# Kernel optimization log

Measured on AMD Instinct MI355X. Metric: run time of the kernel, lower is better.

Reference implementation:

```python
import jax, jax.numpy as jnp
import numpy as np

D_MODEL = 512
BATCH_A = 8192
MAX_MATCHES = 16
N_B = 100000
D_HID = 2 * D_MODEL  # 1024
D_IN = 2 * D_MODEL   # concat([a, mean_b])


def setup_inputs() -> dict:
    key = jax.random.key(0)
    ks = jax.random.split(key, 10)
    table_a_emb = jax.random.normal(ks[0], (BATCH_A, D_MODEL), dtype=jnp.float32)
    table_b_emb = jax.random.normal(ks[1], (N_B, D_MODEL), dtype=jnp.float32)
    # padded neighbor lists; negative values mark padding / no-match
    match_indices = jax.random.randint(ks[2], (BATCH_A, MAX_MATCHES), -5, N_B, dtype=jnp.int64)
    s_in = 1.0 / np.sqrt(D_IN)
    s_h = 1.0 / np.sqrt(D_HID)
    W_in = jax.random.uniform(ks[3], (D_IN, D_HID), jnp.float32, -s_in, s_in)
    b_in = jax.random.uniform(ks[4], (D_HID,), jnp.float32, -s_in, s_in)
    W_h = jax.random.uniform(ks[5], (D_HID, D_HID), jnp.float32, -s_h, s_h)
    b_h = jax.random.uniform(ks[6], (D_HID,), jnp.float32, -s_h, s_h)
    W_out = jax.random.uniform(ks[7], (D_HID, D_MODEL), jnp.float32, -s_h, s_h)
    b_out = jax.random.uniform(ks[8], (D_MODEL,), jnp.float32, -s_h, s_h)
    return {"table_a_emb": table_a_emb, "table_b_emb": table_b_emb,
            "match_indices": match_indices, "W_in": W_in, "b_in": b_in,
            "W_h": W_h, "b_h": b_h, "W_out": W_out, "b_out": b_out}


def reference(table_a_emb, table_b_emb, match_indices, W_in, b_in, W_h, b_h, W_out, b_out):
    mask = match_indices >= 0                                   # [B, M]
    safe_idx = jnp.where(mask, match_indices, 0)
    gathered = table_b_emb[safe_idx] * mask[..., None].astype(table_b_emb.dtype)  # [B, M, D]
    counts = mask.sum(axis=-1)                                  # [B]
    denom = jnp.maximum(counts, 1).astype(table_b_emb.dtype)[:, None]
    agg_b = gathered.sum(axis=1) / denom                        # [B, D] masked mean
    combined = jnp.concatenate([table_a_emb, agg_b], axis=-1)   # [B, 2D]
    h = jax.nn.relu(combined @ W_in + b_in)
    h = jax.nn.relu(h @ W_h + b_h)
    out = h @ W_out + b_out                                     # [B, D]
    # rows with zero valid matches emit zeros, not MLP(concat(a, 0))
    return jnp.where((counts > 0)[:, None], out, jnp.zeros_like(out))
```

## Files before the change

### kernel.cpp

```cpp
#include <hip/hip_runtime.h>

#define DM 512
#define DI 1024
#define MM 16

typedef __attribute__((ext_vector_type(4))) float f32x4;
typedef __attribute__((ext_vector_type(8))) short short8;
typedef __attribute__((ext_vector_type(8))) unsigned short ushort8;

__device__ __forceinline__ unsigned short f2bf(float x) {
  union { float f; unsigned u; } c; c.f = x;
  unsigned r = (c.u + 0x7fffu + ((c.u >> 16) & 1u)) >> 16;
  return (unsigned short)r;
}

__device__ __forceinline__ void gload_lds16(const void* g, void* l) {
  __builtin_amdgcn_global_load_lds(
      (const __attribute__((address_space(1))) unsigned int*)g,
      (__attribute__((address_space(3))) unsigned int*)l, 16, 0, 0);
}

__global__ void wt_bf16_kernel(const float* __restrict__ W,
                               unsigned short* __restrict__ Wt,
                               int K, int N) {
  __shared__ float tile[32][33];
  int bx = blockIdx.x * 32;
  int by = blockIdx.y * 32;
  int tx = threadIdx.x & 31, ty = threadIdx.x >> 5;
  #pragma unroll
  for (int i = ty; i < 32; i += 8)
    tile[i][tx] = W[(size_t)(by + i) * N + bx + tx];
  __syncthreads();
  #pragma unroll
  for (int i = ty; i < 32; i += 8)
    Wt[(size_t)(bx + i) * K + by + tx] = f2bf(tile[tx][i]);
}

__global__ void build_x_kernel(const float* __restrict__ Aemb,
                               const float* __restrict__ Bemb,
                               const int* __restrict__ midx,
                               unsigned short* __restrict__ X,
                               int* __restrict__ counts) {
  int row = blockIdx.x * 4 + (threadIdx.x >> 6);
  int l = threadIdx.x & 63;
  float acc[8] = {0,0,0,0,0,0,0,0};
  int cnt = 0;
  const int* ip = midx + row * MM;
  #pragma unroll
  for (int m = 0; m < MM; ++m) {
    int id = ip[m];
    if (id >= 0) {
      ++cnt;
      const f32x4* p = (const f32x4*)(Bemb + (size_t)id * DM) + l * 2;
      f32x4 u = p[0], v = p[1];
      acc[0]+=u[0]; acc[1]+=u[1]; acc[2]+=u[2]; acc[3]+=u[3];
      acc[4]+=v[0]; acc[5]+=v[1]; acc[6]+=v[2]; acc[7]+=v[3];
    }
  }
  float inv = 1.0f / (float)(cnt > 0 ? cnt : 1);
  const f32x4* pa = (const f32x4*)(Aemb + (size_t)row * DM) + l * 2;
  f32x4 a0 = pa[0], a1 = pa[1];
  ushort8 va, vb;
  va[0]=f2bf(a0[0]); va[1]=f2bf(a0[1]); va[2]=f2bf(a0[2]); va[3]=f2bf(a0[3]);
  va[4]=f2bf(a1[0]); va[5]=f2bf(a1[1]); va[6]=f2bf(a1[2]); va[7]=f2bf(a1[3]);
  #pragma unroll
  for (int i = 0; i < 8; ++i) vb[i] = f2bf(acc[i] * inv);
  *(ushort8*)(X + (size_t)row * DI + l * 8) = va;
  *(ushort8*)(X + (size_t)row * DI + DM + l * 8) = vb;
  if (l == 0) counts[row] = cnt;
}

template<int RELU, int FINAL>
__global__ __launch_bounds__(256, 2)
void gemm_kernel(const unsigned short* __restrict__ A,
                 const unsigned short* __restrict__ Bt,
                 const float* __restrict__ bias,
                 unsigned short* __restrict__ Cb,
                 float* __restrict__ Cf,
                 const int* __restrict__ counts,
                 int M, int N, int K) {
  __shared__ __align__(16) unsigned short As[128 * 64];
  __shared__ __align__(16) unsigned short Bs[128 * 64];
  const int t = threadIdx.x;
  const int l = t & 63, w = t >> 6;
  const int wr = w >> 1, wc = w & 1;
  const int blockM = blockIdx.y * 128, blockN = blockIdx.x * 128;
  const unsigned short* Ab = A + (size_t)blockM * K;
  const unsigned short* Bb = Bt + (size_t)blockN * K;

  f32x4 acc[4][4];
  #pragma unroll
  for (int m = 0; m < 4; ++m)
    #pragma unroll
    for (int n = 0; n < 4; ++n) acc[m][n] = (f32x4){0.f, 0.f, 0.f, 0.f};

  int so_row[4], so_col[4];
  #pragma unroll
  for (int c = 0; c < 4; ++c) {
    int o = c * 4096 + t * 16;
    int row = o >> 7;
    int cb = (o & 127) ^ ((row & 7) << 4);
    so_row[c] = row; so_col[c] = cb >> 1;
  }

  const int r = l & 15, ko = (l >> 4) * 8;
  const int swz = (r & 7) << 4;
  const char* Ac = (const char*)As;
  const char* Bc = (const char*)Bs;
  const int NT = K >> 6;

  #pragma unroll
  for (int c = 0; c < 4; ++c) {
    gload_lds16(Ab + (size_t)so_row[c] * K + so_col[c], (char*)As + c * 4096 + w * 1024);
    gload_lds16(Bb + (size_t)so_row[c] * K + so_col[c], (char*)Bs + c * 4096 + w * 1024);
  }

  for (int kt = 0; kt < NT; ++kt) {
    __syncthreads();
    #pragma unroll
    for (int kk = 0; kk < 64; kk += 32) {
      short8 aF[4], bF[4];
      #pragma unroll
      for (int m = 0; m < 4; ++m) {
        int byteo = ((wr * 64 + m * 16 + r) * 128 + (kk + ko) * 2) ^ swz;
        aF[m] = *(const short8*)(Ac + byteo);
      }
      #pragma unroll
      for (int n = 0; n < 4; ++n) {
        int byteo = ((wc * 64 + n * 16 + r) * 128 + (kk + ko) * 2) ^ swz;
        bF[n] = *(const short8*)(Bc + byteo);
      }
      #pragma unroll
      for (int m = 0; m < 4; ++m)
        #pragma unroll
        for (int n = 0; n < 4; ++n)
          acc[m][n] = __builtin_amdgcn_mfma_f32_16x16x32_bf16(aF[m], bF[n], acc[m][n], 0, 0, 0);
    }
    __syncthreads();
    if (kt + 1 < NT) {
      int k0 = (kt + 1) << 6;
      #pragma unroll
      for (int c = 0; c < 4; ++c) {
        gload_lds16(Ab + (size_t)so_row[c] * K + k0 + so_col[c], (char*)As + c * 4096 + w * 1024);
        gload_lds16(Bb + (size_t)so_row[c] * K + k0 + so_col[c], (char*)Bs + c * 4096 + w * 1024);
      }
    }
  }

  float bn[4];
  #pragma unroll
  for (int n = 0; n < 4; ++n) bn[n] = bias[blockN + wc * 64 + n * 16 + r];
  const int rowBase = blockM + wr * 64 + (l >> 4) * 4;
  #pragma unroll
  for (int m = 0; m < 4; ++m) {
    #pragma unroll
    for (int j = 0; j < 4; ++j) {
      int grow = rowBase + m * 16 + j;
      if (FINAL) {
        float cm = (counts[grow] > 0) ? 1.0f : 0.0f;
        #pragma unroll
        for (int n = 0; n < 4; ++n) {
          float v = (acc[m][n][j] + bn[n]) * cm;
          Cf[(size_t)grow * N + blockN + wc * 64 + n * 16 + r] = v;
        }
      } else {
        #pragma unroll
        for (int n = 0; n < 4; ++n) {
          float v = acc[m][n][j] + bn[n];
          if (RELU) v = v > 0.f ? v : 0.f;
          Cb[(size_t)grow * N + blockN + wc * 64 + n * 16 + r] = f2bf(v);
        }
      }
    }
  }
}

extern "C" void kernel_launch(void* const* d_in, const int* in_sizes, int n_in,
                              void* d_out, int out_size, void* d_ws, size_t ws_size,
                              hipStream_t stream) {
  const float* a_emb = (const float*)d_in[0];
  const float* b_emb = (const float*)d_in[1];
  const int*   midx  = (const int*)d_in[2];
  const float* W_in  = (const float*)d_in[3];
  const float* b_in  = (const float*)d_in[4];
  const float* W_h   = (const float*)d_in[5];
  const float* b_h   = (const float*)d_in[6];
  const float* W_out = (const float*)d_in[7];
  const float* b_out = (const float*)d_in[8];

  char* ws = (char*)d_ws;
  unsigned short* X      = (unsigned short*)(ws);
  unsigned short* H1     = (unsigned short*)(ws + 16777216);
  unsigned short* Wt_in  = (unsigned short*)(ws + 33554432);
  unsigned short* Wt_h   = (unsigned short*)(ws + 35651584);
  unsigned short* Wt_out = (unsigned short*)(ws + 37748736);
  int*            counts = (int*)(ws + 38797312);

  wt_bf16_kernel<<<dim3(32, 32), 256, 0, stream>>>(W_in,  Wt_in,  1024, 1024);
  wt_bf16_kernel<<<dim3(32, 32), 256, 0, stream>>>(W_h,   Wt_h,   1024, 1024);
  wt_bf16_kernel<<<dim3(16, 32), 256, 0, stream>>>(W_out, Wt_out, 1024, 512);
  build_x_kernel<<<2048, 256, 0, stream>>>(a_emb, b_emb, midx, X, counts);

  gemm_kernel<1, 0><<<dim3(8, 64), 256, 0, stream>>>(X,  Wt_in,  b_in,  H1, nullptr, nullptr, 8192, 1024, 1024);
  gemm_kernel<1, 0><<<dim3(8, 64), 256, 0, stream>>>(H1, Wt_h,   b_h,   X,  nullptr, nullptr, 8192, 1024, 1024);
  gemm_kernel<0, 1><<<dim3(4, 64), 256, 0, stream>>>(X,  Wt_out, b_out, nullptr, (float*)d_out, counts, 8192, 512, 1024);
}
```

Before: 129.5 us.

## Fuse weight transpose and gather prep into one kernel; XCD-swizzle GEMM tiles

Merges the three weight-transpose launches and the gather/mean build kernel into a single prep kernel whose block index picks the sub-task, removing three launches and their serialization gaps. The GEMM remaps workgroup IDs so consecutive IDs on the same XCD (wg mod 8) cover contiguous tile regions, which should improve L2 reuse of A and B tiles. It also uses readfirstlane on the row index so it is treated as uniform. The fused kernel mixes heterogeneous block types, and the swizzle assumes the workgroup count divides by 8.

Result: faster. 114.5 us (-11.6%).

```diff
diff --git a/kernel.cpp b/kernel.cpp
--- a/kernel.cpp
+++ b/kernel.cpp
@@ -20,13 +20,11 @@
       (__attribute__((address_space(3))) unsigned int*)l, 16, 0, 0);
 }
 
-__global__ void wt_bf16_kernel(const float* __restrict__ W,
-                               unsigned short* __restrict__ Wt,
-                               int K, int N) {
-  __shared__ float tile[32][33];
-  int bx = blockIdx.x * 32;
-  int by = blockIdx.y * 32;
-  int tx = threadIdx.x & 31, ty = threadIdx.x >> 5;
+
+__device__ __forceinline__ void wt_tile(const float* __restrict__ W,
+                                        unsigned short* __restrict__ Wt,
+                                        int K, int N, int bx, int by,
+                                        float (*tile)[33], int tx, int ty) {
   #pragma unroll
   for (int i = ty; i < 32; i += 8)
     tile[i][tx] = W[(size_t)(by + i) * N + bx + tx];
@@ -36,12 +34,34 @@
     Wt[(size_t)(bx + i) * K + by + tx] = f2bf(tile[tx][i]);
 }
 
-__global__ void build_x_kernel(const float* __restrict__ Aemb,
-                               const float* __restrict__ Bemb,
-                               const int* __restrict__ midx,
-                               unsigned short* __restrict__ X,
-                               int* __restrict__ counts) {
-  int row = blockIdx.x * 4 + (threadIdx.x >> 6);
+__global__ __launch_bounds__(256)
+void prep_kernel(const float* __restrict__ Aemb,
+                 const float* __restrict__ Bemb,
+                 const int* __restrict__ midx,
+                 const float* __restrict__ W_in,
+                 const float* __restrict__ W_h,
+                 const float* __restrict__ W_out,
+                 unsigned short* __restrict__ X,
+                 int* __restrict__ counts,
+                 unsigned short* __restrict__ Wt_in,
+                 unsigned short* __restrict__ Wt_h,
+                 unsigned short* __restrict__ Wt_out) {
+  __shared__ float tile[32][33];
+  const int b = blockIdx.x;
+  const int tx = threadIdx.x & 31, ty = threadIdx.x >> 5;
+  if (b < 1024) {
+    wt_tile(W_in, Wt_in, 1024, 1024, (b & 31) * 32, (b >> 5) * 32, tile, tx, ty);
+    return;
+  } else if (b < 2048) {
+    int lb = b - 1024;
+    wt_tile(W_h, Wt_h, 1024, 1024, (lb & 31) * 32, (lb >> 5) * 32, tile, tx, ty);
+    return;
+  } else if (b < 2560) {
+    int lb = b - 2048;
+    wt_tile(W_out, Wt_out, 1024, 512, (lb & 15) * 32, (lb >> 4) * 32, tile, tx, ty);
+    return;
+  }
+  int row = __builtin_amdgcn_readfirstlane((b - 2560) * 4 + (threadIdx.x >> 6));
   int l = threadIdx.x & 63;
   float acc[8] = {0,0,0,0,0,0,0,0};
   int cnt = 0;
@@ -84,7 +104,13 @@
   const int t = threadIdx.x;
   const int l = t & 63, w = t >> 6;
   const int wr = w >> 1, wc = w & 1;
-  const int blockM = blockIdx.y * 128, blockN = blockIdx.x * 128;
+
+  const int nwg = gridDim.x * gridDim.y;
+  const int wg = blockIdx.y * gridDim.x + blockIdx.x;
+  const int swzid = (wg & 7) * (nwg >> 3) + (wg >> 3);
+  const int bx = swzid % gridDim.x, by = swzid / gridDim.x;
+
+  const int blockM = by * 128, blockN = bx * 128;
   const unsigned short* Ab = A + (size_t)blockM * K;
   const unsigned short* Bb = Bt + (size_t)blockN * K;
 
@@ -196,10 +222,8 @@
   unsigned short* Wt_out = (unsigned short*)(ws + 37748736);
   int*            counts = (int*)(ws + 38797312);
 
-  wt_bf16_kernel<<<dim3(32, 32), 256, 0, stream>>>(W_in,  Wt_in,  1024, 1024);
-  wt_bf16_kernel<<<dim3(32, 32), 256, 0, stream>>>(W_h,   Wt_h,   1024, 1024);
-  wt_bf16_kernel<<<dim3(16, 32), 256, 0, stream>>>(W_out, Wt_out, 1024, 512);
-  build_x_kernel<<<2048, 256, 0, stream>>>(a_emb, b_emb, midx, X, counts);
+  prep_kernel<<<4608, 256, 0, stream>>>(a_emb, b_emb, midx, W_in, W_h, W_out,
+                                        X, counts, Wt_in, Wt_h, Wt_out);
 
   gemm_kernel<1, 0><<<dim3(8, 64), 256, 0, stream>>>(X,  Wt_in,  b_in,  H1, nullptr, nullptr, 8192, 1024, 1024);
   gemm_kernel<1, 0><<<dim3(8, 64), 256, 0, stream>>>(H1, Wt_h,   b_h,   X,  nullptr, nullptr, 8192, 1024, 1024);
```
